# Optimization experiments

Measured on AMD Instinct MI355X. Metric: run time of the kernel, lower is better.

## Reference

```python
import jax, jax.numpy as jnp
import numpy as np

NUM_EMBEDDINGS = 1024
EMBEDDING_DIM = 64
COMMIT_COST = 0.25


def setup_inputs() -> dict:
    key = jax.random.key(0)
    k1, k2 = jax.random.split(key)
    latent = jax.random.normal(k1, (32, EMBEDDING_DIM, 32, 32), dtype=jnp.float32)
    embedding_weight = jax.random.normal(k2, (NUM_EMBEDDINGS, EMBEDDING_DIM), dtype=jnp.float32)
    return {"latent": latent, "embedding_weight": embedding_weight}


def reference(latent, embedding_weight):
    # rearrange 'b n j d -> b j d n'; n == embedding_dim
    lat = jnp.transpose(latent, (0, 2, 3, 1))  # [b, j, d, n]
    flat = lat.reshape(-1, EMBEDDING_DIM)      # [T, D]
    # squared-euclidean distances [T, K]
    distances = (
        jnp.sum(flat ** 2, axis=1, keepdims=True)
        + jnp.sum(embedding_weight ** 2, axis=1)
        - 2.0 * flat @ embedding_weight.T
    )
    idx = jnp.argmin(distances, axis=1)                         # [T]
    encodings = jax.nn.one_hot(idx, NUM_EMBEDDINGS, dtype=flat.dtype)  # [T, K]
    quantized_flat = embedding_weight[idx]                      # gather == encodings @ W
    quantized = quantized_flat.reshape(lat.shape)               # [b, j, d, n]

    e_latent_loss = jnp.mean((jax.lax.stop_gradient(quantized) - lat) ** 2)
    loss = COMMIT_COST * e_latent_loss

    # straight-through estimator
    quantized_st = lat + jax.lax.stop_gradient(quantized - lat)

    avg_probs = jnp.mean(encodings, axis=0)
    perplexity = jnp.exp(-jnp.sum(avg_probs * jnp.log(avg_probs + 1e-10)))

    # rearrange back 'b j d n -> b n j d'
    quantized_out = jnp.transpose(quantized_st, (0, 3, 1, 2))
    return quantized_out, loss, perplexity, encodings, distances
```

## Files before the change

kernel.cpp:

```cpp
#include <hip/hip_runtime.h>
#include <cfloat>

#define T_TOTAL 32768
#define DIM 64
#define KCODES 1024

static constexpr long long OFF_Q    = 0;
static constexpr long long OFF_LOSS = 2097152;
static constexpr long long OFF_PERP = 2097153;
static constexpr long long OFF_ENC  = 2097154;
static constexpr long long OFF_DIST = 2097154LL + 33554432LL;


#define AS1 __attribute__((address_space(1)))
#define AS3 __attribute__((address_space(3)))

__device__ __forceinline__ void gld16(const float* g, float* l) {
    __builtin_amdgcn_global_load_lds((const AS1 unsigned int*)g,
                                     (AS3 unsigned int*)l, 16, 0, 0);
}

#define PHASE_SYNC(N) do {                                        \
    asm volatile("s_waitcnt vmcnt(" #N ")" ::: "memory");         \
    __builtin_amdgcn_s_barrier();                                 \
    __builtin_amdgcn_sched_barrier(0);                            \
} while (0)

__global__ __launch_bounds__(256) void vq_prep_kernel(const float* __restrict__ W,
                                                      float* __restrict__ ww,
                                                      float* __restrict__ WT,
                                                      float* __restrict__ out,
                                                      int* __restrict__ counts,
                                                      float* __restrict__ lossSum) {
    const int tid = threadIdx.x;
    const int b   = blockIdx.x;
    if (b < 256) {
        const int lane = tid & 63;
        const int code = b * 4 + (tid >> 6);
        float v = W[code * DIM + lane];
        float s = v * v;
        #pragma unroll
        for (int off = 32; off > 0; off >>= 1)
            s += __shfl_down(s, off, 64);
        if (lane == 0) ww[code] = s;
    } else if (b < 320) {
        const int n = b - 256;
        #pragma unroll
        for (int i = 0; i < 4; ++i) {
            int k = i * 256 + tid;
            WT[n * KCODES + k] = W[k * DIM + n];
        }
    } else if (b < 384) {
        float* __restrict__ enc = out + OFF_ENC;
        const float2 z2 = make_float2(0.f, 0.f);
        const int r0 = (b - 320) * 512 + tid * 2;
        const long long rb = (long long)r0 * KCODES;
        *(float2*)&enc[rb]               = z2;
        *(float2*)&enc[rb + 1022]        = z2;
        *(float2*)&enc[rb + 1024]        = z2;
        *(float2*)&enc[rb + 1024 + 1022] = z2;
    } else {
        #pragma unroll
        for (int i = 0; i < 4; ++i) counts[i * 256 + tid] = 0;
        if (tid == 0) lossSum[0] = 0.f;
    }
}

__global__ __launch_bounds__(256, 2) void vq_main_kernel(const float* __restrict__ lat,
                                                         const float* __restrict__ W,
                                                         const float* __restrict__ ww,
                                                         const float* __restrict__ WT,
                                                         float* __restrict__ out,
                                                         int* __restrict__ counts,
                                                         float* __restrict__ lossSum) {
    __shared__ float xT[64 * 64];
    __shared__ float wS[2][8 * 512];
    __shared__ float wwS[KCODES];
    __shared__ float xx[64];
    __shared__ int   selIdx[64];

    const int tid = threadIdx.x;
    const int tx  = tid & 31;
    const int ty  = tid >> 5;
    const int t0  = blockIdx.x * 64;
    const long long base = (long long)(t0 >> 10) * 65536 + (long long)(t0 & 1023);
    const int wbase = (tid & 192) * 4;

    #pragma unroll
    for (int i = 0; i < 4; ++i) {
        const int e = i * 256 + tid;
        gld16(&lat[base + (long long)(e >> 4) * 1024 + (e & 15) * 4],
              &xT[i * 1024 + wbase]);
    }
    #pragma unroll
    for (int i = 0; i < 4; ++i) {
        const int e = i * 256 + tid;
        gld16(&WT[(e >> 7) * KCODES + (e & 127) * 4],
              &wS[0][i * 1024 + wbase]);
    }
    *(float4*)&wwS[tid * 4] = *(const float4*)&ww[tid * 4];
    __syncthreads();

    if (tid < 64) {
        float s = 0.f;
        #pragma unroll 8
        for (int n = 0; n < 64; ++n) {
            float v = xT[n * 64 + tid];
            s = fmaf(v, v, s);
        }
        xx[tid] = s;
    }

    float minV[8];
    int   minI[8];
    #pragma unroll
    for (int r = 0; r < 8; ++r) { minV[r] = FLT_MAX; minI[r] = 0; }

    float acc[8][16];
    float* __restrict__ distOut = out + OFF_DIST;
    float* __restrict__ enc     = out + OFF_ENC;
    const float4 z4 = make_float4(0.f, 0.f, 0.f, 0.f);
    const int tcl = (tid < 255 ? tid : 254) * 4;

    for (int p = 0; p < 16; ++p) {
        const int c   = p >> 3;
        const int q   = p & 7;
        const int buf = p & 1;

        if (p < 15) {
            const int pn = p + 1;
            const float* srcb = WT + (pn & 7) * (8 * KCODES) + (pn >> 3) * 512;
            float* dstb = &wS[pn & 1][0];
            #pragma unroll
            for (int i = 0; i < 4; ++i) {
                const int e = i * 256 + tid;
                gld16(&srcb[(e >> 7) * KCODES + (e & 127) * 4],
                      &dstb[i * 1024 + wbase]);
            }
        }
        asm volatile("" ::: "memory");

        {
            float* pz = enc + (long long)(t0 + p * 4) * KCODES + 2;
            *(float4*)(pz + tcl)        = z4;
            *(float4*)(pz + 1024 + tcl) = z4;
            *(float4*)(pz + 2048 + tcl) = z4;
            *(float4*)(pz + 3072 + tcl) = z4;
        }

        if (q == 0) {
            #pragma unroll
            for (int r = 0; r < 8; ++r)
                #pragma unroll
                for (int k = 0; k < 16; ++k) acc[r][k] = 0.f;
        }

        #pragma unroll 2
        for (int nn = 0; nn < 8; ++nn) {
            const float* xrow = &xT[(q * 8 + nn) * 64];
            const float* wrow = &wS[buf][nn * 512];
            float4 a0 = *(const float4*)&xrow[ty * 4];
            float4 a1 = *(const float4*)&xrow[32 + ty * 4];
            float4 b0 = *(const float4*)&wrow[tx * 4];
            float4 b1 = *(const float4*)&wrow[128 + tx * 4];
            float4 b2 = *(const float4*)&wrow[256 + tx * 4];
            float4 b3 = *(const float4*)&wrow[384 + tx * 4];
            float ar[8]  = {a0.x, a0.y, a0.z, a0.w, a1.x, a1.y, a1.z, a1.w};
            float br[16] = {b0.x, b0.y, b0.z, b0.w, b1.x, b1.y, b1.z, b1.w,
                            b2.x, b2.y, b2.z, b2.w, b3.x, b3.y, b3.z, b3.w};
            #pragma unroll
            for (int r = 0; r < 8; ++r)
                #pragma unroll
                for (int k = 0; k < 16; ++k)
                    acc[r][k] = fmaf(ar[r], br[k], acc[r][k]);
        }

        if (q == 7) {
            const int kb = c * 512 + tx * 4;
            float wr[16];
            #pragma unroll
            for (int qq = 0; qq < 4; ++qq) {
                float4 w4 = *(const float4*)&wwS[kb + qq * 128];
                wr[qq*4+0] = w4.x; wr[qq*4+1] = w4.y; wr[qq*4+2] = w4.z; wr[qq*4+3] = w4.w;
            }
            #pragma unroll
            for (int r = 0; r < 8; ++r) {
                const int row = (r >> 2) * 32 + ty * 4 + (r & 3);
                const float xxr = xx[row];
                const long long ro = (long long)(t0 + row) * KCODES + kb;
                #pragma unroll
                for (int qq = 0; qq < 4; ++qq) {
                    float d0 = (xxr + wr[qq*4+0]) - 2.f * acc[r][qq*4+0];
                    float d1 = (xxr + wr[qq*4+1]) - 2.f * acc[r][qq*4+1];
                    float d2 = (xxr + wr[qq*4+2]) - 2.f * acc[r][qq*4+2];
                    float d3 = (xxr + wr[qq*4+3]) - 2.f * acc[r][qq*4+3];
                    const int k0 = kb + qq * 128;
                    if (d0 < minV[r]) { minV[r] = d0; minI[r] = k0;     }
                    if (d1 < minV[r]) { minV[r] = d1; minI[r] = k0 + 1; }
                    if (d2 < minV[r]) { minV[r] = d2; minI[r] = k0 + 2; }
                    if (d3 < minV[r]) { minV[r] = d3; minI[r] = k0 + 3; }
                    *(float2*)&distOut[ro + qq * 128]     = make_float2(d0, d1);
                    *(float2*)&distOut[ro + qq * 128 + 2] = make_float2(d2, d3);
                }
            }
        }

        if (q == 7) PHASE_SYNC(63);
        else        PHASE_SYNC(4);
    }

    float* wSf  = &wS[0][0];
    float* redV = wSf;
    int*   redI = (int*)(wSf + 64 * 33);
    #pragma unroll
    for (int r = 0; r < 8; ++r) {
        const int row = (r >> 2) * 32 + ty * 4 + (r & 3);
        redV[row * 33 + tx] = minV[r];
        redI[row * 33 + tx] = minI[r];
    }
    __syncthreads();
    if (tid < 64) {
        float best = redV[tid * 33];
        int   bi   = redI[tid * 33];
        #pragma unroll
        for (int s = 1; s < 32; ++s) {
            float v  = redV[tid * 33 + s];
            int   i2 = redI[tid * 33 + s];
            if (v < best || (v == best && i2 < bi)) { best = v; bi = i2; }
        }
        selIdx[tid] = bi;
        atomicAdd(&counts[bi], 1);
    }
    __syncthreads();

    float* qS = wSf;
    #pragma unroll
    for (int i = 0; i < 16; ++i) {
        int e   = i * 256 + tid;
        int row = e >> 6;
        int n   = e & 63;
        qS[row * 65 + n] = W[selIdx[row] * DIM + n];
    }
    __syncthreads();

    float ls = 0.f;
    #pragma unroll
    for (int i = 0; i < 4; ++i) {
        int e2  = i * 256 + tid;
        int n   = e2 >> 4;
        int tl0 = (e2 & 15) * 4;
        float q0 = qS[(tl0 + 0) * 65 + n];
        float q1 = qS[(tl0 + 1) * 65 + n];
        float q2 = qS[(tl0 + 2) * 65 + n];
        float q3 = qS[(tl0 + 3) * 65 + n];
        float x0 = xT[n * 64 + tl0 + 0];
        float x1 = xT[n * 64 + tl0 + 1];
        float x2 = xT[n * 64 + tl0 + 2];
        float x3 = xT[n * 64 + tl0 + 3];
        *(float4*)&out[OFF_Q + base + (long long)n * 1024 + tl0] = make_float4(q0, q1, q2, q3);
        float e0 = q0 - x0; ls = fmaf(e0, e0, ls);
        float e1 = q1 - x1; ls = fmaf(e1, e1, ls);
        float e2d = q2 - x2; ls = fmaf(e2d, e2d, ls);
        float e3 = q3 - x3; ls = fmaf(e3, e3, ls);
    }
    #pragma unroll
    for (int off = 32; off > 0; off >>= 1)
        ls += __shfl_down(ls, off, 64);
    if ((tid & 63) == 0) atomicAdd(lossSum, ls);

    if (tid < 64)
        enc[(long long)(t0 + tid) * KCODES + selIdx[tid]] = 1.f;
}

__global__ __launch_bounds__(1024) void vq_finalize_kernel(const int* __restrict__ counts,
                                                           const float* __restrict__ lossSum,
                                                           float* __restrict__ out) {
    __shared__ float red[16];
    const int tid = threadIdx.x;
    float p = (float)counts[tid] * (1.0f / 32768.0f);
    float term = p * logf(p + 1e-10f);
    #pragma unroll
    for (int off = 32; off > 0; off >>= 1)
        term += __shfl_down(term, off, 64);
    if ((tid & 63) == 0) red[tid >> 6] = term;
    __syncthreads();
    if (tid == 0) {
        float s = 0.f;
        #pragma unroll
        for (int i = 0; i < 16; ++i) s += red[i];
        out[OFF_PERP] = expf(-s);
        out[OFF_LOSS] = 0.25f * lossSum[0] * (1.0f / 2097152.0f);
    }
}

extern "C" void kernel_launch(void* const* d_in, const int* in_sizes, int n_in,
                              void* d_out, int out_size, void* d_ws, size_t ws_size,
                              hipStream_t stream) {
    (void)in_sizes; (void)n_in; (void)out_size; (void)ws_size;
    const float* lat = (const float*)d_in[0];
    const float* W   = (const float*)d_in[1];
    float* out = (float*)d_out;

    int*   counts  = (int*)d_ws;
    float* ww      = (float*)((char*)d_ws + 4096);
    float* lossSum = (float*)((char*)d_ws + 8192);
    float* WT      = (float*)((char*)d_ws + 12288);

    vq_prep_kernel<<<385, 256, 0, stream>>>(W, ww, WT, out, counts, lossSum);
    vq_main_kernel<<<512, 256, 0, stream>>>(lat, W, ww, WT, out, counts, lossSum);
    vq_finalize_kernel<<<1, 1024, 0, stream>>>(counts, lossSum, out);
}
```

Measured before the change: 338.0 us.

## Double threads per block, halve per-thread tile, use shuffle argmin reduction

The main VQ kernel now runs 512 threads per block, so each thread accumulates an 8x8 distance tile instead of 8x16, and the cooperative loads, encoding-zero stores and wait counts are rescaled to match. The cross-thread argmin moves from an LDS scratch pass plus a serial scan to wave-level xor shuffles, with one lane per row writing the selected index. The aim is to raise occupancy and memory-level parallelism for the store-heavy distance and encoding writes, and to cut the reduction cost. In exchange it adds more per-block barrier participants and uses smaller register tiles with lower reuse per LDS load.

```diff
diff --git a/kernel.cpp b/kernel.cpp
--- a/kernel.cpp
+++ b/kernel.cpp
@@ -66,7 +66,7 @@
     }
 }
 
-__global__ __launch_bounds__(256, 2) void vq_main_kernel(const float* __restrict__ lat,
+__global__ __launch_bounds__(512, 4) void vq_main_kernel(const float* __restrict__ lat,
                                                          const float* __restrict__ W,
                                                          const float* __restrict__ ww,
                                                          const float* __restrict__ WT,
@@ -80,25 +80,25 @@
     __shared__ int   selIdx[64];
 
     const int tid = threadIdx.x;
-    const int tx  = tid & 31;
-    const int ty  = tid >> 5;
+    const int tx  = tid & 63;
+    const int ty  = tid >> 6;
     const int t0  = blockIdx.x * 64;
     const long long base = (long long)(t0 >> 10) * 65536 + (long long)(t0 & 1023);
-    const int wbase = (tid & 192) * 4;
-
-    #pragma unroll
-    for (int i = 0; i < 4; ++i) {
-        const int e = i * 256 + tid;
+    const int wbase = (tid & 448) * 4;
+
+    #pragma unroll
+    for (int i = 0; i < 2; ++i) {
+        const int e = i * 512 + tid;
         gld16(&lat[base + (long long)(e >> 4) * 1024 + (e & 15) * 4],
-              &xT[i * 1024 + wbase]);
-    }
-    #pragma unroll
-    for (int i = 0; i < 4; ++i) {
-        const int e = i * 256 + tid;
+              &xT[i * 2048 + wbase]);
+    }
+    #pragma unroll
+    for (int i = 0; i < 2; ++i) {
+        const int e = i * 512 + tid;
         gld16(&WT[(e >> 7) * KCODES + (e & 127) * 4],
-              &wS[0][i * 1024 + wbase]);
-    }
-    *(float4*)&wwS[tid * 4] = *(const float4*)&ww[tid * 4];
+              &wS[0][i * 2048 + wbase]);
+    }
+    *(float2*)&wwS[tid * 2] = *(const float2*)&ww[tid * 2];
     __syncthreads();
 
     if (tid < 64) {
@@ -116,11 +116,10 @@
     #pragma unroll
     for (int r = 0; r < 8; ++r) { minV[r] = FLT_MAX; minI[r] = 0; }
 
-    float acc[8][16];
+    float acc[8][8];
     float* __restrict__ distOut = out + OFF_DIST;
     float* __restrict__ enc     = out + OFF_ENC;
     const float4 z4 = make_float4(0.f, 0.f, 0.f, 0.f);
-    const int tcl = (tid < 255 ? tid : 254) * 4;
 
     for (int p = 0; p < 16; ++p) {
         const int c   = p >> 3;
@@ -132,27 +131,28 @@
             const float* srcb = WT + (pn & 7) * (8 * KCODES) + (pn >> 3) * 512;
             float* dstb = &wS[pn & 1][0];
             #pragma unroll
-            for (int i = 0; i < 4; ++i) {
-                const int e = i * 256 + tid;
+            for (int i = 0; i < 2; ++i) {
+                const int e = i * 512 + tid;
                 gld16(&srcb[(e >> 7) * KCODES + (e & 127) * 4],
-                      &dstb[i * 1024 + wbase]);
+                      &dstb[i * 2048 + wbase]);
             }
         }
         asm volatile("" ::: "memory");
 
         {
-            float* pz = enc + (long long)(t0 + p * 4) * KCODES + 2;
-            *(float4*)(pz + tcl)        = z4;
-            *(float4*)(pz + 1024 + tcl) = z4;
-            *(float4*)(pz + 2048 + tcl) = z4;
-            *(float4*)(pz + 3072 + tcl) = z4;
+            float4* pzf = (float4*)(enc + (long long)(t0 + p * 4) * KCODES + 2);
+            const int rr = tid >> 7;
+            const int j  = tid & 127;
+            const int j2 = (j + 128 > 254) ? 254 : j + 128;
+            pzf[rr * 256 + j]  = z4;
+            pzf[rr * 256 + j2] = z4;
         }
 
         if (q == 0) {
             #pragma unroll
             for (int r = 0; r < 8; ++r)
                 #pragma unroll
-                for (int k = 0; k < 16; ++k) acc[r][k] = 0.f;
+                for (int k = 0; k < 8; ++k) acc[r][k] = 0.f;
         }
 
         #pragma unroll 2
@@ -162,26 +162,24 @@
             float4 a0 = *(const float4*)&xrow[ty * 4];
             float4 a1 = *(const float4*)&xrow[32 + ty * 4];
             float4 b0 = *(const float4*)&wrow[tx * 4];
-            float4 b1 = *(const float4*)&wrow[128 + tx * 4];
-            float4 b2 = *(const float4*)&wrow[256 + tx * 4];
-            float4 b3 = *(const float4*)&wrow[384 + tx * 4];
-            float ar[8]  = {a0.x, a0.y, a0.z, a0.w, a1.x, a1.y, a1.z, a1.w};
-            float br[16] = {b0.x, b0.y, b0.z, b0.w, b1.x, b1.y, b1.z, b1.w,
-                            b2.x, b2.y, b2.z, b2.w, b3.x, b3.y, b3.z, b3.w};
+            float4 b1 = *(const float4*)&wrow[256 + tx * 4];
+            float ar[8] = {a0.x, a0.y, a0.z, a0.w, a1.x, a1.y, a1.z, a1.w};
+            float br[8] = {b0.x, b0.y, b0.z, b0.w, b1.x, b1.y, b1.z, b1.w};
             #pragma unroll
             for (int r = 0; r < 8; ++r)
                 #pragma unroll
-                for (int k = 0; k < 16; ++k)
+                for (int k = 0; k < 8; ++k)
                     acc[r][k] = fmaf(ar[r], br[k], acc[r][k]);
         }
 
         if (q == 7) {
             const int kb = c * 512 + tx * 4;
-            float wr[16];
-            #pragma unroll
-            for (int qq = 0; qq < 4; ++qq) {
-                float4 w4 = *(const float4*)&wwS[kb + qq * 128];
-                wr[qq*4+0] = w4.x; wr[qq*4+1] = w4.y; wr[qq*4+2] = w4.z; wr[qq*4+3] = w4.w;
+            float wr[8];
+            {
+                float4 wa = *(const float4*)&wwS[kb];
+                float4 wb = *(const float4*)&wwS[kb + 256];
+                wr[0]=wa.x; wr[1]=wa.y; wr[2]=wa.z; wr[3]=wa.w;
+                wr[4]=wb.x; wr[5]=wb.y; wr[6]=wb.z; wr[7]=wb.w;
             }
             #pragma unroll
             for (int r = 0; r < 8; ++r) {
@@ -189,54 +187,48 @@
                 const float xxr = xx[row];
                 const long long ro = (long long)(t0 + row) * KCODES + kb;
                 #pragma unroll
-                for (int qq = 0; qq < 4; ++qq) {
-                    float d0 = (xxr + wr[qq*4+0]) - 2.f * acc[r][qq*4+0];
-                    float d1 = (xxr + wr[qq*4+1]) - 2.f * acc[r][qq*4+1];
-                    float d2 = (xxr + wr[qq*4+2]) - 2.f * acc[r][qq*4+2];
-                    float d3 = (xxr + wr[qq*4+3]) - 2.f * acc[r][qq*4+3];
-                    const int k0 = kb + qq * 128;
+                for (int g = 0; g < 2; ++g) {
+                    float d0 = (xxr + wr[g*4+0]) - 2.f * acc[r][g*4+0];
+                    float d1 = (xxr + wr[g*4+1]) - 2.f * acc[r][g*4+1];
+                    float d2 = (xxr + wr[g*4+2]) - 2.f * acc[r][g*4+2];
+                    float d3 = (xxr + wr[g*4+3]) - 2.f * acc[r][g*4+3];
+                    const int k0 = kb + g * 256;
                     if (d0 < minV[r]) { minV[r] = d0; minI[r] = k0;     }
                     if (d1 < minV[r]) { minV[r] = d1; minI[r] = k0 + 1; }
                     if (d2 < minV[r]) { minV[r] = d2; minI[r] = k0 + 2; }
                     if (d3 < minV[r]) { minV[r] = d3; minI[r] = k0 + 3; }
-                    *(float2*)&distOut[ro + qq * 128]     = make_float2(d0, d1);
-                    *(float2*)&distOut[ro + qq * 128 + 2] = make_float2(d2, d3);
+                    *(float2*)&distOut[ro + g * 256]     = make_float2(d0, d1);
+                    *(float2*)&distOut[ro + g * 256 + 2] = make_float2(d2, d3);
                 }
             }
         }
 
-        if (q == 7) PHASE_SYNC(63);
-        else        PHASE_SYNC(4);
-    }
-
-    float* wSf  = &wS[0][0];
-    float* redV = wSf;
-    int*   redI = (int*)(wSf + 64 * 33);
+        if (q == 7) PHASE_SYNC(34);
+        else        PHASE_SYNC(2);
+    }
+
     #pragma unroll
     for (int r = 0; r < 8; ++r) {
-        const int row = (r >> 2) * 32 + ty * 4 + (r & 3);
-        redV[row * 33 + tx] = minV[r];
-        redI[row * 33 + tx] = minI[r];
+        float v  = minV[r];
+        int   bi = minI[r];
+        #pragma unroll
+        for (int off = 1; off < 64; off <<= 1) {
+            float v2 = __shfl_xor(v, off, 64);
+            int   i2 = __shfl_xor(bi, off, 64);
+            if (v2 < v || (v2 == v && i2 < bi)) { v = v2; bi = i2; }
+        }
+        if (tx == r) {
+            const int row = (r >> 2) * 32 + ty * 4 + (r & 3);
+            selIdx[row] = bi;
+            atomicAdd(&counts[bi], 1);
+        }
     }
     __syncthreads();
-    if (tid < 64) {
-        float best = redV[tid * 33];
-        int   bi   = redI[tid * 33];
-        #pragma unroll
-        for (int s = 1; s < 32; ++s) {
-            float v  = redV[tid * 33 + s];
-            int   i2 = redI[tid * 33 + s];
-            if (v < best || (v == best && i2 < bi)) { best = v; bi = i2; }
-        }
-        selIdx[tid] = bi;
-        atomicAdd(&counts[bi], 1);
-    }
-    __syncthreads();
-
-    float* qS = wSf;
-    #pragma unroll
-    for (int i = 0; i < 16; ++i) {
-        int e   = i * 256 + tid;
+
+    float* qS = &wS[0][0];
+    #pragma unroll
+    for (int i = 0; i < 8; ++i) {
+        int e   = i * 512 + tid;
         int row = e >> 6;
         int n   = e & 63;
         qS[row * 65 + n] = W[selIdx[row] * DIM + n];
@@ -245,8 +237,8 @@
 
     float ls = 0.f;
     #pragma unroll
-    for (int i = 0; i < 4; ++i) {
-        int e2  = i * 256 + tid;
+    for (int i = 0; i < 2; ++i) {
+        int e2  = i * 512 + tid;
         int n   = e2 >> 4;
         int tl0 = (e2 & 15) * 4;
         float q0 = qS[(tl0 + 0) * 65 + n];
@@ -266,7 +258,7 @@
     #pragma unroll
     for (int off = 32; off > 0; off >>= 1)
         ls += __shfl_down(ls, off, 64);
-    if ((tid & 63) == 0) atomicAdd(lossSum, ls);
+    if (tx == 0) atomicAdd(lossSum, ls);
 
     if (tid < 64)
         enc[(long long)(t0 + tid) * KCODES + selIdx[tid]] = 1.f;
@@ -307,6 +299,6 @@
     float* WT      = (float*)((char*)d_ws + 12288);
 
     vq_prep_kernel<<<385, 256, 0, stream>>>(W, ww, WT, out, counts, lossSum);
-    vq_main_kernel<<<512, 256, 0, stream>>>(lat, W, ww, WT, out, counts, lossSum);
+    vq_main_kernel<<<512, 512, 0, stream>>>(lat, W, ww, WT, out, counts, lossSum);
     vq_finalize_kernel<<<1, 1024, 0, stream>>>(counts, lossSum, out);
 }
```

Result: slower. 401.7 us (+18.9%).
